# Optimization experiments

Hardware: AMD Instinct MI355X
Metric: run time of the kernel (lower is better)

## Reference

```python
import jax, jax.numpy as jnp
import numpy as np

N_AGENTS, OBS_DIM, HID, ACT_DIM = 8192, 64, 128, 16


def setup_inputs() -> dict:
    key = jax.random.key(0)
    k = jax.random.split(key, 8)
    obs_agents = jax.random.normal(k[0], (N_AGENTS, OBS_DIM), dtype=jnp.float32)
    # binary adjacency, {0,1}, int32 (index/mask semantics, non-differentiable)
    adj = jax.random.randint(k[1], (N_AGENTS, N_AGENTS), 0, 2, dtype=jnp.int32)
    def lin(kk, fan_in, fan_out):
        lim = 1.0 / np.sqrt(fan_in)
        kw, kb = jax.random.split(kk)
        W = jax.random.uniform(kw, (fan_in, fan_out), jnp.float32, -lim, lim)
        b = jax.random.uniform(kb, (fan_out,), jnp.float32, -lim, lim)
        return W, b
    W1, b1 = lin(k[2], OBS_DIM, HID)          # encoder
    W2, b2 = lin(k[3], 2 * HID, HID)          # actor layer 1
    W3, b3 = lin(k[4], HID, ACT_DIM)          # actor layer 2
    return {"obs_agents": obs_agents, "adj": adj,
            "W1": W1, "b1": b1, "W2": W2, "b2": b2, "W3": W3, "b3": b3}


def reference(obs_agents, adj, W1, b1, W2, b2, W3, b3):
    # per-agent encode: h = tanh(obs @ W1 + b1)  -> [N, HID]
    h = jnp.tanh(obs_agents @ W1 + b1)
    # neighbor mean message: mean of h[j] over j with adj[i,j]!=0, zeros if no neighbors
    a = adj.astype(h.dtype)                      # [N, N] binary
    deg = jnp.sum(a, axis=1, keepdims=True)      # [N, 1]
    msg = (a @ h) / jnp.maximum(deg, 1.0)        # zero rows stay zero
    # actor MLP on concat([h, msg])
    combined = jnp.concatenate([h, msg], axis=-1)            # [N, 2*HID]
    hid = jnp.tanh(combined @ W2 + b2)                        # [N, HID]
    logits = hid @ W3 + b3                                    # [N, ACT_DIM]
    return logits
```

## Files before the change

### kernel.cpp

```cpp
#include <hip/hip_runtime.h>
#include <stdint.h>
#include <math.h>

#define NAG 8192
#define NB  144
#define LDA 72
#define LDB 72

typedef __attribute__((ext_vector_type(8))) short short8;
typedef __attribute__((ext_vector_type(4))) float floatx4;

__device__ __forceinline__ float bf2f(unsigned short u) {
    union { uint32_t i; float f; } v; v.i = ((uint32_t)u) << 16; return v.f;
}
__device__ __forceinline__ unsigned short f2bf(float f) {
    union { float f; uint32_t i; } v; v.f = f;
    uint32_t x = v.i;
    return (unsigned short)((x + 0x7FFFu + ((x >> 16) & 1u)) >> 16);
}

__global__ __launch_bounds__(256) void k0_init(
    float* __restrict__ C, int* __restrict__ flag,
    const unsigned short* __restrict__ W1raw)
{
    size_t i = ((size_t)blockIdx.x * 256 + threadIdx.x) * 4;
    *reinterpret_cast<float4*>(C + i) = make_float4(0.f, 0.f, 0.f, 0.f);
    if (blockIdx.x == 0 && threadIdx.x < 64) {
        int big = 0;
        #pragma unroll
        for (int j = 0; j < 8; ++j) {
            float v = bf2f(W1raw[threadIdx.x * 8 + j]);
            if (!(fabsf(v) <= 1e6f)) big = 1;
        }
        unsigned long long m = __ballot(big);
        if (threadIdx.x == 0) *flag = (m != 0ull) ? 1 : 0;
    }
}

__global__ __launch_bounds__(256) void k1_encode(
    const void* __restrict__ obs,
    const void* __restrict__ W1,
    const void* __restrict__ b1,
    const int* __restrict__ flag,
    float* __restrict__ h_f32,
    unsigned short* __restrict__ hT)
{
    __shared__ float obs_lds[32][68];
    __shared__ unsigned short ht_lds[128][33];
    const int t = threadIdx.x;
    const int abase = blockIdx.x * 32;
    const bool isf = (*flag != 0);

    {
        int a = t >> 3, c0 = (t & 7) * 8;
        if (isf) {
            const float* p = (const float*)obs;
            #pragma unroll
            for (int j = 0; j < 8; ++j)
                obs_lds[a][c0 + j] = p[(size_t)(abase + a) * 64 + c0 + j];
        } else {
            const unsigned short* p = (const unsigned short*)obs;
            #pragma unroll
            for (int j = 0; j < 8; ++j)
                obs_lds[a][c0 + j] = bf2f(p[(size_t)(abase + a) * 64 + c0 + j]);
        }
    }
    __syncthreads();

    const int o = t & 127;
    const int half = t >> 7;
    float acc[16];
    if (isf) {
        const float* Wp = (const float*)W1;
        float bias = ((const float*)b1)[o];
        #pragma unroll
        for (int i = 0; i < 16; ++i) acc[i] = bias;
        for (int k0 = 0; k0 < 64; k0 += 8) {
            float w[8];
            #pragma unroll
            for (int j = 0; j < 8; ++j) w[j] = Wp[(k0 + j) * 128 + o];
            #pragma unroll
            for (int j = 0; j < 8; ++j)
                #pragma unroll
                for (int i = 0; i < 16; ++i)
                    acc[i] = fmaf(obs_lds[half * 16 + i][k0 + j], w[j], acc[i]);
        }
    } else {
        const unsigned short* Wp = (const unsigned short*)W1;
        float bias = bf2f(((const unsigned short*)b1)[o]);
        #pragma unroll
        for (int i = 0; i < 16; ++i) acc[i] = bias;
        for (int k0 = 0; k0 < 64; k0 += 8) {
            float w[8];
            #pragma unroll
            for (int j = 0; j < 8; ++j) w[j] = bf2f(Wp[(k0 + j) * 128 + o]);
            #pragma unroll
            for (int j = 0; j < 8; ++j)
                #pragma unroll
                for (int i = 0; i < 16; ++i)
                    acc[i] = fmaf(obs_lds[half * 16 + i][k0 + j], w[j], acc[i]);
        }
    }
    #pragma unroll
    for (int i = 0; i < 16; ++i) {
        float th = tanhf(acc[i]);
        int a = half * 16 + i;
        h_f32[(size_t)(abase + a) * 128 + o] = th;
        ht_lds[o][a] = f2bf(th);
    }
    __syncthreads();

    for (int p = 0; p < 18; ++p) {
        int n = p * 8 + (t >> 5);
        int a = t & 31;
        unsigned short v;
        if (n < 128)       v = ht_lds[n][a];
        else if (n == 128) v = 0x3F80;
        else               v = 0;
        hT[(size_t)n * NAG + abase + a] = v;
    }
}

__global__ __launch_bounds__(256, 4) void k2_msggemm(
    const int* __restrict__ adj,
    const unsigned short* __restrict__ hT,
    float* __restrict__ C)
{
    __shared__ __align__(16) unsigned short Alds[64 * LDA];
    __shared__ __align__(16) unsigned short Blds[NB * LDB];
    const int t = threadIdx.x;
    const int mtile = blockIdx.x & 127;
    const int ks = blockIdx.x >> 7;
    const int row0 = mtile * 64;
    const int kbeg = ks * 1024;

    const int wave = t >> 6, lane = t & 63;
    const int fm = lane & 15, quad = lane >> 4;

    floatx4 acc[9];
    #pragma unroll
    for (int i = 0; i < 9; ++i) acc[i] = (floatx4)0.f;

    const int ar = t >> 2, aq = t & 3;
    const int bln = t & 7, brow = t >> 3;

    const int* aPtr = adj + (size_t)(row0 + ar) * NAG;
    int4 aReg[4];
    uint4 bReg[5];

    #pragma unroll
    for (int i = 0; i < 4; ++i)
        aReg[i] = *reinterpret_cast<const int4*>(aPtr + kbeg + i * 16 + aq * 4);
    #pragma unroll
    for (int p = 0; p < 5; ++p) {
        int n = p * 32 + brow;
        if (n < NB)
            bReg[p] = *reinterpret_cast<const uint4*>(hT + (size_t)n * NAG + kbeg + bln * 8);
    }

    for (int it = 0; it < 16; ++it) {
        __syncthreads();
        #pragma unroll
        for (int i = 0; i < 4; ++i) {
            int c = i * 16 + aq * 4;
            uint32_t d0 = ((uint32_t)aReg[i].x | ((uint32_t)aReg[i].y << 16)) * 0x3F80u;
            uint32_t d1 = ((uint32_t)aReg[i].z | ((uint32_t)aReg[i].w << 16)) * 0x3F80u;
            *reinterpret_cast<uint2*>(&Alds[ar * LDA + c]) = make_uint2(d0, d1);
        }
        #pragma unroll
        for (int p = 0; p < 5; ++p) {
            int n = p * 32 + brow;
            if (n < NB)
                *reinterpret_cast<uint4*>(&Blds[n * LDB + bln * 8]) = bReg[p];
        }
        __syncthreads();
        if (it < 15) {
            int kb = kbeg + (it + 1) * 64;
            #pragma unroll
            for (int i = 0; i < 4; ++i)
                aReg[i] = *reinterpret_cast<const int4*>(aPtr + kb + i * 16 + aq * 4);
            #pragma unroll
            for (int p = 0; p < 5; ++p) {
                int n = p * 32 + brow;
                if (n < NB)
                    bReg[p] = *reinterpret_cast<const uint4*>(hT + (size_t)n * NAG + kb + bln * 8);
            }
        }
        #pragma unroll
        for (int kk = 0; kk < 64; kk += 32) {
            short8 af = *reinterpret_cast<const short8*>(&Alds[(wave * 16 + fm) * LDA + kk + quad * 8]);
            #pragma unroll
            for (int nt = 0; nt < 9; ++nt) {
                short8 bf = *reinterpret_cast<const short8*>(&Blds[(nt * 16 + fm) * LDB + kk + quad * 8]);
                acc[nt] = __builtin_amdgcn_mfma_f32_16x16x32_bf16(af, bf, acc[nt], 0, 0, 0);
            }
        }
    }
    #pragma unroll
    for (int nt = 0; nt < 9; ++nt) {
        int col = nt * 16 + fm;
        #pragma unroll
        for (int r = 0; r < 4; ++r) {
            int row = row0 + wave * 16 + quad * 4 + r;
            atomicAdd(&C[(size_t)row * NB + col], acc[nt][r]);
        }
    }
}

__global__ __launch_bounds__(256) void k3_actor(
    const float* __restrict__ h_f32,
    const float* __restrict__ C,
    const void* __restrict__ W2,
    const void* __restrict__ b2,
    const void* __restrict__ W3,
    const void* __restrict__ b3,
    const int* __restrict__ flag,
    void* __restrict__ out)
{
    __shared__ float comb[32][256];
    __shared__ float hid[32][132];
    __shared__ float inv_lds[32];
    const int t = threadIdx.x;
    const int abase = blockIdx.x * 32;
    const bool isf = (*flag != 0);

    if (t < 32) {
        float deg = C[(size_t)(abase + t) * NB + 128];
        inv_lds[t] = 1.0f / fmaxf(deg, 1.0f);
    }
    __syncthreads();
    #pragma unroll
    for (int j = 0; j < 4; ++j) {
        int idx = j * 256 + t, a = idx >> 5, c = idx & 31;
        float4 v = *reinterpret_cast<const float4*>(h_f32 + (size_t)(abase + a) * 128 + c * 4);
        *reinterpret_cast<float4*>(&comb[a][c * 4]) = v;
    }
    #pragma unroll
    for (int j = 0; j < 4; ++j) {
        int idx = j * 256 + t, a = idx >> 5, c = idx & 31;
        float4 v = *reinterpret_cast<const float4*>(C + (size_t)(abase + a) * NB + c * 4);
        float s = inv_lds[a];
        v.x *= s; v.y *= s; v.z *= s; v.w *= s;
        *reinterpret_cast<float4*>(&comb[a][128 + c * 4]) = v;
    }
    __syncthreads();

    const int o = t & 127, half = t >> 7;
    float acc[16];
    if (isf) {
        const float* Wp = (const float*)W2;
        float bias = ((const float*)b2)[o];
        #pragma unroll
        for (int i = 0; i < 16; ++i) acc[i] = bias;
        for (int c0 = 0; c0 < 256; c0 += 8) {
            float w[8];
            #pragma unroll
            for (int j = 0; j < 8; ++j) w[j] = Wp[(c0 + j) * 128 + o];
            #pragma unroll
            for (int j = 0; j < 8; ++j)
                #pragma unroll
                for (int i = 0; i < 16; ++i)
                    acc[i] = fmaf(comb[half * 16 + i][c0 + j], w[j], acc[i]);
        }
    } else {
        const unsigned short* Wp = (const unsigned short*)W2;
        float bias = bf2f(((const unsigned short*)b2)[o]);
        #pragma unroll
        for (int i = 0; i < 16; ++i) acc[i] = bias;
        for (int c0 = 0; c0 < 256; c0 += 8) {
            float w[8];
            #pragma unroll
            for (int j = 0; j < 8; ++j) w[j] = bf2f(Wp[(c0 + j) * 128 + o]);
            #pragma unroll
            for (int j = 0; j < 8; ++j)
                #pragma unroll
                for (int i = 0; i < 16; ++i)
                    acc[i] = fmaf(comb[half * 16 + i][c0 + j], w[j], acc[i]);
        }
    }
    #pragma unroll
    for (int i = 0; i < 16; ++i)
        hid[half * 16 + i][o] = tanhf(acc[i]);
    __syncthreads();

    const int q = t & 15, ar = t >> 4;
    float l0, l1;
    if (isf) {
        const float* Wp = (const float*)W3;
        l0 = ((const float*)b3)[q]; l1 = l0;
        #pragma unroll 4
        for (int oo = 0; oo < 128; ++oo) {
            float w = Wp[oo * 16 + q];
            l0 = fmaf(hid[ar][oo], w, l0);
            l1 = fmaf(hid[ar + 16][oo], w, l1);
        }
    } else {
        const unsigned short* Wp = (const unsigned short*)W3;
        l0 = bf2f(((const unsigned short*)b3)[q]); l1 = l0;
        #pragma unroll 4
        for (int oo = 0; oo < 128; ++oo) {
            float w = bf2f(Wp[oo * 16 + q]);
            l0 = fmaf(hid[ar][oo], w, l0);
            l1 = fmaf(hid[ar + 16][oo], w, l1);
        }
    }
    size_t i0 = (size_t)(abase + ar) * 16 + q;
    size_t i1 = (size_t)(abase + ar + 16) * 16 + q;
    if (isf) {
        ((float*)out)[i0] = l0;
        ((float*)out)[i1] = l1;
    } else {
        ((unsigned short*)out)[i0] = f2bf(l0);
        ((unsigned short*)out)[i1] = f2bf(l1);
    }
}

extern "C" void kernel_launch(void* const* d_in, const int* in_sizes, int n_in,
                              void* d_out, int out_size, void* d_ws, size_t ws_size,
                              hipStream_t stream) {
    const void* obs = d_in[0];
    const int*  adj = (const int*)d_in[1];
    const void* W1  = d_in[2];
    const void* b1  = d_in[3];
    const void* W2  = d_in[4];
    const void* b2  = d_in[5];
    const void* W3  = d_in[6];
    const void* b3  = d_in[7];

    char* ws = (char*)d_ws;
    unsigned short* hT = (unsigned short*)(ws);
    float* h_f32 = (float*)(ws + 2359296);
    float* C     = (float*)(ws + 2359296 + 4194304);
    int*   flag  = (int*)(ws + 2359296 + 4194304 + 4718592);

    hipLaunchKernelGGL(k0_init, dim3(1152), dim3(256), 0, stream, C, flag, (const unsigned short*)W1);
    hipLaunchKernelGGL(k1_encode, dim3(256), dim3(256), 0, stream, obs, W1, b1, flag, h_f32, hT);
    hipLaunchKernelGGL(k2_msggemm, dim3(1024), dim3(256), 0, stream, adj, hT, C);
    hipLaunchKernelGGL(k3_actor, dim3(256), dim3(256), 0, stream, h_f32, C, W2, b2, W3, b3, flag, d_out);
}
```

Before: 515.5 us.

## Replace atomic split-K reduction with per-split partial buffers and retile message GEMM

The adjacency GEMM now uses 32-row M tiles with 4 K splits of 2048 instead of 64-row tiles with 8 splits. Each split writes plain stores into its own partial buffer rather than doing atomicAdd into a zeroed C. The actor kernel sums the 4 partials, which removes the large zeroing pass in the init kernel. The GEMM loop also double-buffers the A register loads across two iterations. In exchange, each hT (B) tile is reloaded for twice as many M tiles, the waves split the output columns unevenly (5 and 4 tiles), and the workspace grows to hold 4 partial buffers.

New measurement: 652.2 us. 1.27x slower.

```diff
diff --git a/kernel.cpp b/kernel.cpp
--- a/kernel.cpp
+++ b/kernel.cpp
@@ -4,8 +4,10 @@
 
 #define NAG 8192
 #define NB  144
+#define BM  32
 #define LDA 72
 #define LDB 72
+#define NSPLIT 4
 
 typedef __attribute__((ext_vector_type(8))) short short8;
 typedef __attribute__((ext_vector_type(4))) float floatx4;
@@ -19,22 +21,17 @@
     return (unsigned short)((x + 0x7FFFu + ((x >> 16) & 1u)) >> 16);
 }
 
-__global__ __launch_bounds__(256) void k0_init(
-    float* __restrict__ C, int* __restrict__ flag,
-    const unsigned short* __restrict__ W1raw)
+__global__ __launch_bounds__(64) void k0_init(
+    int* __restrict__ flag, const unsigned short* __restrict__ W1raw)
 {
-    size_t i = ((size_t)blockIdx.x * 256 + threadIdx.x) * 4;
-    *reinterpret_cast<float4*>(C + i) = make_float4(0.f, 0.f, 0.f, 0.f);
-    if (blockIdx.x == 0 && threadIdx.x < 64) {
-        int big = 0;
-        #pragma unroll
-        for (int j = 0; j < 8; ++j) {
-            float v = bf2f(W1raw[threadIdx.x * 8 + j]);
-            if (!(fabsf(v) <= 1e6f)) big = 1;
-        }
-        unsigned long long m = __ballot(big);
-        if (threadIdx.x == 0) *flag = (m != 0ull) ? 1 : 0;
-    }
+    int big = 0;
+    #pragma unroll
+    for (int j = 0; j < 8; ++j) {
+        float v = bf2f(W1raw[threadIdx.x * 8 + j]);
+        if (!(fabsf(v) <= 1e6f)) big = 1;
+    }
+    unsigned long long m = __ballot(big);
+    if (threadIdx.x == 0) *flag = (m != 0ull) ? 1 : 0;
 }
 
 __global__ __launch_bounds__(256) void k1_encode(
@@ -124,92 +121,113 @@
 __global__ __launch_bounds__(256, 4) void k2_msggemm(
     const int* __restrict__ adj,
     const unsigned short* __restrict__ hT,
-    float* __restrict__ C)
+    float* __restrict__ Cpart)
 {
-    __shared__ __align__(16) unsigned short Alds[64 * LDA];
+    __shared__ __align__(16) unsigned short Alds[BM * LDA];
     __shared__ __align__(16) unsigned short Blds[NB * LDB];
     const int t = threadIdx.x;
-    const int mtile = blockIdx.x & 127;
-    const int ks = blockIdx.x >> 7;
-    const int row0 = mtile * 64;
-    const int kbeg = ks * 1024;
+    const int mtile = blockIdx.x & 255;
+    const int ks = blockIdx.x >> 8;
+    const int row0 = mtile * BM;
+    const int kbeg = ks * 2048;
 
     const int wave = t >> 6, lane = t & 63;
     const int fm = lane & 15, quad = lane >> 4;
-
-    floatx4 acc[9];
-    #pragma unroll
-    for (int i = 0; i < 9; ++i) acc[i] = (floatx4)0.f;
-
-    const int ar = t >> 2, aq = t & 3;
+    const int mh = (wave >> 1) * 16;
+    const int ntbase = (wave & 1) * 5;
+    const int ntc = (wave & 1) ? 4 : 5;
+
+    floatx4 acc[5];
+    #pragma unroll
+    for (int i = 0; i < 5; ++i) acc[i] = (floatx4)0.f;
+
+    const int ar = t >> 3, aq = t & 7;
     const int bln = t & 7, brow = t >> 3;
 
-    const int* aPtr = adj + (size_t)(row0 + ar) * NAG;
-    int4 aReg[4];
-    uint4 bReg[5];
-
-    #pragma unroll
-    for (int i = 0; i < 4; ++i)
-        aReg[i] = *reinterpret_cast<const int4*>(aPtr + kbeg + i * 16 + aq * 4);
-    #pragma unroll
-    for (int p = 0; p < 5; ++p) {
-        int n = p * 32 + brow;
-        if (n < NB)
-            bReg[p] = *reinterpret_cast<const uint4*>(hT + (size_t)n * NAG + kbeg + bln * 8);
-    }
-
-    for (int it = 0; it < 16; ++it) {
+    const int* aP = adj + (size_t)(row0 + ar) * NAG + aq * 8;
+    int4 rA0[2], rA1[2];
+    uint4 rB[5];
+
+#define LOADA(R, K) do { \
+        (R)[0] = *reinterpret_cast<const int4*>(aP + (K));      \
+        (R)[1] = *reinterpret_cast<const int4*>(aP + (K) + 4);  \
+    } while (0)
+#define LOADB(K) do { \
+        _Pragma("unroll") \
+        for (int p = 0; p < 5; ++p) { \
+            int n = p * 32 + brow; \
+            if (n < NB) rB[p] = *reinterpret_cast<const uint4*>(hT + (size_t)n * NAG + (K) + bln * 8); \
+        } \
+    } while (0)
+#define STOREA(R) do { \
+        _Pragma("unroll") \
+        for (int c = 0; c < 2; ++c) { \
+            uint32_t d0 = ((uint32_t)(R)[c].x | ((uint32_t)(R)[c].y << 16)) * 0x3F80u; \
+            uint32_t d1 = ((uint32_t)(R)[c].z | ((uint32_t)(R)[c].w << 16)) * 0x3F80u; \
+            *reinterpret_cast<uint2*>(&Alds[ar * LDA + aq * 8 + c * 4]) = make_uint2(d0, d1); \
+        } \
+    } while (0)
+#define STOREB() do { \
+        _Pragma("unroll") \
+        for (int p = 0; p < 5; ++p) { \
+            int n = p * 32 + brow; \
+            if (n < NB) *reinterpret_cast<uint4*>(&Blds[n * LDB + bln * 8]) = rB[p]; \
+        } \
+    } while (0)
+#define COMPUTE() do { \
+        _Pragma("unroll") \
+        for (int kk = 0; kk < 64; kk += 32) { \
+            short8 af = *reinterpret_cast<const short8*>(&Alds[(mh + fm) * LDA + kk + quad * 8]); \
+            for (int j = 0; j < ntc; ++j) { \
+                short8 bf = *reinterpret_cast<const short8*>(&Blds[((ntbase + j) * 16 + fm) * LDB + kk + quad * 8]); \
+                acc[j] = __builtin_amdgcn_mfma_f32_16x16x32_bf16(af, bf, acc[j], 0, 0, 0); \
+            } \
+        } \
+    } while (0)
+
+    LOADA(rA0, kbeg);
+    LOADA(rA1, kbeg + 64);
+    LOADB(kbeg);
+
+    for (int it = 0; it < 32; it += 2) {
         __syncthreads();
-        #pragma unroll
-        for (int i = 0; i < 4; ++i) {
-            int c = i * 16 + aq * 4;
-            uint32_t d0 = ((uint32_t)aReg[i].x | ((uint32_t)aReg[i].y << 16)) * 0x3F80u;
-            uint32_t d1 = ((uint32_t)aReg[i].z | ((uint32_t)aReg[i].w << 16)) * 0x3F80u;
-            *reinterpret_cast<uint2*>(&Alds[ar * LDA + c]) = make_uint2(d0, d1);
-        }
-        #pragma unroll
-        for (int p = 0; p < 5; ++p) {
-            int n = p * 32 + brow;
-            if (n < NB)
-                *reinterpret_cast<uint4*>(&Blds[n * LDB + bln * 8]) = bReg[p];
-        }
+        STOREA(rA0);
+        STOREB();
         __syncthreads();
-        if (it < 15) {
-            int kb = kbeg + (it + 1) * 64;
-            #pragma unroll
-            for (int i = 0; i < 4; ++i)
-                aReg[i] = *reinterpret_cast<const int4*>(aPtr + kb + i * 16 + aq * 4);
-            #pragma unroll
-            for (int p = 0; p < 5; ++p) {
-                int n = p * 32 + brow;
-                if (n < NB)
-                    bReg[p] = *reinterpret_cast<const uint4*>(hT + (size_t)n * NAG + kb + bln * 8);
+        if (it + 1 < 32) LOADB(kbeg + (it + 1) * 64);
+        if (it + 2 < 32) LOADA(rA0, kbeg + (it + 2) * 64);
+        COMPUTE();
+        __syncthreads();
+        STOREA(rA1);
+        STOREB();
+        __syncthreads();
+        if (it + 2 < 32) LOADB(kbeg + (it + 2) * 64);
+        if (it + 3 < 32) LOADA(rA1, kbeg + (it + 3) * 64);
+        COMPUTE();
+    }
+
+    float* out = Cpart + (size_t)ks * (NAG * NB);
+    #pragma unroll
+    for (int j = 0; j < 5; ++j) {
+        if (j < ntc) {
+            int col = (ntbase + j) * 16 + fm;
+            #pragma unroll
+            for (int r = 0; r < 4; ++r) {
+                int row = row0 + mh + quad * 4 + r;
+                out[(size_t)row * NB + col] = acc[j][r];
             }
         }
-        #pragma unroll
-        for (int kk = 0; kk < 64; kk += 32) {
-            short8 af = *reinterpret_cast<const short8*>(&Alds[(wave * 16 + fm) * LDA + kk + quad * 8]);
-            #pragma unroll
-            for (int nt = 0; nt < 9; ++nt) {
-                short8 bf = *reinterpret_cast<const short8*>(&Blds[(nt * 16 + fm) * LDB + kk + quad * 8]);
-                acc[nt] = __builtin_amdgcn_mfma_f32_16x16x32_bf16(af, bf, acc[nt], 0, 0, 0);
-            }
-        }
-    }
-    #pragma unroll
-    for (int nt = 0; nt < 9; ++nt) {
-        int col = nt * 16 + fm;
-        #pragma unroll
-        for (int r = 0; r < 4; ++r) {
-            int row = row0 + wave * 16 + quad * 4 + r;
-            atomicAdd(&C[(size_t)row * NB + col], acc[nt][r]);
-        }
-    }
+    }
+#undef LOADA
+#undef LOADB
+#undef STOREA
+#undef STOREB
+#undef COMPUTE
 }
 
 __global__ __launch_bounds__(256) void k3_actor(
     const float* __restrict__ h_f32,
-    const float* __restrict__ C,
+    const float* __restrict__ Cpart,
     const void* __restrict__ W2,
     const void* __restrict__ b2,
     const void* __restrict__ W3,
@@ -223,9 +241,13 @@
     const int t = threadIdx.x;
     const int abase = blockIdx.x * 32;
     const bool isf = (*flag != 0);
+    const size_t PS = (size_t)NAG * NB;
 
     if (t < 32) {
-        float deg = C[(size_t)(abase + t) * NB + 128];
+        float deg = 0.f;
+        #pragma unroll
+        for (int s = 0; s < NSPLIT; ++s)
+            deg += Cpart[s * PS + (size_t)(abase + t) * NB + 128];
         inv_lds[t] = 1.0f / fmaxf(deg, 1.0f);
     }
     __syncthreads();
@@ -238,9 +260,14 @@
     #pragma unroll
     for (int j = 0; j < 4; ++j) {
         int idx = j * 256 + t, a = idx >> 5, c = idx & 31;
-        float4 v = *reinterpret_cast<const float4*>(C + (size_t)(abase + a) * NB + c * 4);
-        float s = inv_lds[a];
-        v.x *= s; v.y *= s; v.z *= s; v.w *= s;
+        float4 v = make_float4(0.f, 0.f, 0.f, 0.f);
+        #pragma unroll
+        for (int s = 0; s < NSPLIT; ++s) {
+            float4 p = *reinterpret_cast<const float4*>(Cpart + s * PS + (size_t)(abase + a) * NB + c * 4);
+            v.x += p.x; v.y += p.y; v.z += p.z; v.w += p.w;
+        }
+        float sc = inv_lds[a];
+        v.x *= sc; v.y *= sc; v.z *= sc; v.w *= sc;
         *reinterpret_cast<float4*>(&comb[a][128 + c * 4]) = v;
     }
     __syncthreads();
@@ -330,11 +357,11 @@
     char* ws = (char*)d_ws;
     unsigned short* hT = (unsigned short*)(ws);
     float* h_f32 = (float*)(ws + 2359296);
-    float* C     = (float*)(ws + 2359296 + 4194304);
-    int*   flag  = (int*)(ws + 2359296 + 4194304 + 4718592);
-
-    hipLaunchKernelGGL(k0_init, dim3(1152), dim3(256), 0, stream, C, flag, (const unsigned short*)W1);
+    float* Cpart = (float*)(ws + 2359296 + 4194304);
+    int*   flag  = (int*)(ws + 2359296 + 4194304 + 18874368);
+
+    hipLaunchKernelGGL(k0_init, dim3(1), dim3(64), 0, stream, flag, (const unsigned short*)W1);
     hipLaunchKernelGGL(k1_encode, dim3(256), dim3(256), 0, stream, obs, W1, b1, flag, h_f32, hT);
-    hipLaunchKernelGGL(k2_msggemm, dim3(1024), dim3(256), 0, stream, adj, hT, C);
-    hipLaunchKernelGGL(k3_actor, dim3(256), dim3(256), 0, stream, h_f32, C, W2, b2, W3, b3, flag, d_out);
-}
+    hipLaunchKernelGGL(k2_msggemm, dim3(1024), dim3(256), 0, stream, adj, hT, Cpart);
+    hipLaunchKernelGGL(k3_actor, dim3(256), dim3(256), 0, stream, h_f32, Cpart, W2, b2, W3, b3, flag, d_out);
+}
```
